# Performance work log

Hardware: AMD Instinct MI355X
Metric: run time of the kernel (lower is better)

The kernel has to match this reference:

```python
import jax, jax.numpy as jnp
import numpy as np

EPS = 1e-5

def _conv1x1(x, w, b):
    # x: [B, Cin, L], w: [Cout, Cin], b: [Cout]
    return jnp.einsum('oc,bcl->bol', w, x) + b[None, :, None]

def _bn(x, g, b):
    # BatchNorm1d in training mode: batch stats over (B, L), biased variance
    m = jnp.mean(x, axis=(0, 2), keepdims=True)
    v = jnp.var(x, axis=(0, 2), keepdims=True)
    return g[None, :, None] * (x - m) * jax.lax.rsqrt(v + EPS) + b[None, :, None]

def setup_inputs() -> dict:
    key = jax.random.key(0)
    ks = jax.random.split(key, 16)
    B, H, L, K = 32, 32, 32768, 7
    rel, im, out = H // 16, H // 8, H // 4          # 2, 4, 8
    cat = (1 + K) * rel                              # 16
    w = lambda k, shape: jax.random.normal(k, shape, jnp.float32) * 0.1
    return {
        'x': jax.random.normal(ks[0], (B, H, L), jnp.float32),
        'w_phi': w(ks[1], (rel, H)),  'b_phi': w(ks[2], (rel,)),
        'w_psi': w(ks[3], (rel, H)),  'b_psi': w(ks[4], (rel,)),
        'w_beta': w(ks[5], (out, H)), 'b_beta': w(ks[6], (out,)),
        'w_cw1': w(ks[7], (im, cat)), 'b_cw1': w(ks[8], (im,)),
        'w_cw2': w(ks[9], (out, im)), 'b_cw2': w(ks[10], (out,)),
        'w_out': w(ks[11], (H, out)), 'b_out': w(ks[12], (H,)),
        'g_cat': jnp.ones((cat,), jnp.float32),  'be_cat': jnp.zeros((cat,), jnp.float32),
        'g_im': jnp.ones((im,), jnp.float32),    'be_im': jnp.zeros((im,), jnp.float32),
        'g_aggr': jnp.ones((out,), jnp.float32), 'be_aggr': jnp.zeros((out,), jnp.float32),
        'g_hid': jnp.ones((H,), jnp.float32),    'be_hid': jnp.zeros((H,), jnp.float32),
        'kernel_size': 7,
    }

def reference(x, w_phi, b_phi, w_psi, b_psi, w_beta, b_beta,
              w_cw1, b_cw1, w_cw2, b_cw2, w_out, b_out,
              g_cat, be_cat, g_im, be_im, g_aggr, be_aggr, g_hid, be_hid,
              kernel_size):
    B, H, L = x.shape
    phi = _conv1x1(x, w_phi, b_phi)                       # [B, rel, L]
    psi = _conv1x1(x, w_psi, b_psi)                       # [B, rel, L]
    p = kernel_size // 2
    psi_pad = jnp.pad(psi, ((0, 0), (0, 0), (p, p)))
    # F.unfold with kernel (k,1): channel index = c*k + j -> stack kernel axis after channel
    psi_unf = jnp.stack([psi_pad[:, :, j:j + L] for j in range(kernel_size)], axis=2)
    psi_unf = psi_unf.reshape(B, psi.shape[1] * kernel_size, L)   # [B, rel*k, L]
    h = jnp.concatenate([phi, psi_unf], axis=1)           # [B, (1+k)*rel, L]
    h = jax.nn.relu(_bn(h, g_cat, be_cat))
    h = _conv1x1(h, w_cw1, b_cw1)
    h = jax.nn.relu(_bn(h, g_im, be_im))
    weight = _conv1x1(h, w_cw2, b_cw2)                    # [B, out, L]
    beta = _conv1x1(x, w_beta, b_beta)                    # [B, out, L]
    aggr = jax.nn.relu(_bn(weight * beta, g_aggr, be_aggr))
    y = x + _conv1x1(aggr, w_out, b_out)
    return jax.nn.relu(_bn(y, g_hid, be_hid))
```

## Files before the change

### kernel.cpp

```cpp
#include <hip/hip_runtime.h>
#include <math.h>

#define Bn 32
#define Hc 32
#define Ln 32768
#define RELC 2
#define IMC 4
#define OC 8
#define CATC 16
#define KS 7
#define NPOS (Bn*Ln)
#define TPB 256
#define VPT 4
#define PPB (TPB*VPT)
#define TILES (Ln/PPB)
#define NBLK (Bn*TILES)
#define NSLOT 8
#define SSTR 128

#define iS_PHI  0
#define iSS_PHI 2
#define iS_PSI  4
#define iSS_PSI 6
#define iS_T    8
#define iSS_T   12
#define iS_AP   16
#define iSS_AP  24
#define iS_Y    32
#define iSS_Y   64
#define bPF  0
#define bPFS 6
#define bQL  12
#define bQLS 18
#define NBST 24

#define FMA4(A,S,V) { A.x=fmaf((S),(V).x,A.x); A.y=fmaf((S),(V).y,A.y); A.z=fmaf((S),(V).z,A.z); A.w=fmaf((S),(V).w,A.w); }

__device__ inline float4 affrelu(float4 v, float a, float d){
    float4 r;
    r.x=fmaxf(fmaf(a,v.x,d),0.f); r.y=fmaxf(fmaf(a,v.y,d),0.f);
    r.z=fmaxf(fmaf(a,v.z,d),0.f); r.w=fmaxf(fmaf(a,v.w,d),0.f);
    return r;
}
__device__ inline double wredd(double v){
    #pragma unroll
    for (int o=32;o>0;o>>=1) v += __shfl_down(v,o,64);
    return v;
}
__device__ inline float wredf(float v){
    #pragma unroll
    for (int o=32;o>0;o>>=1) v += __shfl_down(v,o,64);
    return v;
}
__device__ inline void atomAddD(double* p, double v){ unsafeAtomicAdd(p, v); }

__global__ void __launch_bounds__(TPB) k1(
    const float* __restrict__ x,
    const float* __restrict__ w_phi, const float* __restrict__ b_phi,
    const float* __restrict__ w_psi, const float* __restrict__ b_psi,
    const float* __restrict__ w_beta,const float* __restrict__ b_beta,
    float* __restrict__ phi, float* __restrict__ psi, float* __restrict__ beta,
    double* __restrict__ stats, double* __restrict__ bstats)
{
    __shared__ __align__(16) float wl[Hc*12 + 12];
    __shared__ double rbuf[4][8];
    const int tid = threadIdx.x;
    for (int i = tid; i < Hc*12; i += TPB) {
        int h = i/12, j = i%12;
        float v;
        if (j < 2)      v = w_phi[j*Hc + h];
        else if (j < 4) v = w_psi[(j-2)*Hc + h];
        else            v = w_beta[(j-4)*Hc + h];
        wl[h*12 + j] = v;
    }
    if (tid < 12)
        wl[Hc*12+tid] = (tid<2) ? b_phi[tid] : (tid<4) ? b_psi[tid-2] : b_beta[tid-4];
    __syncthreads();

    const int b    = blockIdx.x / TILES;
    const int tile = blockIdx.x % TILES;
    const int l0   = tile*PPB + tid*VPT;
    double* st = stats + (size_t)(blockIdx.x & (NSLOT-1))*SSTR;

    float4 acc[12];
    #pragma unroll
    for (int j=0;j<12;++j){ float bb = wl[Hc*12+j]; acc[j]=make_float4(bb,bb,bb,bb); }

    const float* xb = x + (size_t)b*Hc*Ln + l0;
    #pragma unroll 4
    for (int h=0; h<Hc; ++h) {
        const float4 xv = *(const float4*)(xb + (size_t)h*Ln);
        const float4 w0 = *(const float4*)(&wl[h*12+0]);
        const float4 w1 = *(const float4*)(&wl[h*12+4]);
        const float4 w2 = *(const float4*)(&wl[h*12+8]);
        FMA4(acc[0],w0.x,xv); FMA4(acc[1],w0.y,xv); FMA4(acc[2],w0.z,xv); FMA4(acc[3],w0.w,xv);
        FMA4(acc[4],w1.x,xv); FMA4(acc[5],w1.y,xv); FMA4(acc[6],w1.z,xv); FMA4(acc[7],w1.w,xv);
        FMA4(acc[8],w2.x,xv); FMA4(acc[9],w2.y,xv); FMA4(acc[10],w2.z,xv); FMA4(acc[11],w2.w,xv);
    }
    #pragma unroll
    for (int c=0;c<RELC;++c) *(float4*)(phi + ((size_t)(b*RELC+c))*Ln + l0) = acc[c];
    #pragma unroll
    for (int c=0;c<RELC;++c) *(float4*)(psi + ((size_t)(b*RELC+c))*Ln + l0) = acc[2+c];
    #pragma unroll
    for (int o=0;o<OC;++o)   *(float4*)(beta + ((size_t)(b*OC+o))*Ln + l0)  = acc[4+o];

    double vals[8];
    #pragma unroll
    for (int c=0;c<2;++c){
        float4 v = acc[c];
        vals[c]   = (double)v.x+v.y+v.z+v.w;
        vals[2+c] = (double)v.x*v.x+(double)v.y*v.y+(double)v.z*v.z+(double)v.w*v.w;
        float4 u = acc[2+c];
        vals[4+c] = (double)u.x+u.y+u.z+u.w;
        vals[6+c] = (double)u.x*u.x+(double)u.y*u.y+(double)u.z*u.z+(double)u.w*u.w;
    }
    if (tile==0 || tile==TILES-1) {
        #pragma unroll
        for (int c=0;c<2;++c){
            const float pv[4] = {acc[2+c].x, acc[2+c].y, acc[2+c].z, acc[2+c].w};
            #pragma unroll
            for (int e=0;e<4;++e){
                int le = l0+e;
                if (le < 3) {
                    atomAddD(&bstats[bPF +c*3+le], (double)pv[e]);
                    atomAddD(&bstats[bPFS+c*3+le], (double)pv[e]*pv[e]);
                }
                if (le >= Ln-3) {
                    int i = le-(Ln-3);
                    atomAddD(&bstats[bQL +c*3+i], (double)pv[e]);
                    atomAddD(&bstats[bQLS+c*3+i], (double)pv[e]*pv[e]);
                }
            }
        }
    }
    const int lane=tid&63, wid=tid>>6;
    #pragma unroll
    for (int i=0;i<8;++i){ double r=wredd(vals[i]); if(lane==0) rbuf[wid][i]=r; }
    __syncthreads();
    if (tid<8) atomAddD(&st[iS_PHI+tid], rbuf[0][tid]+rbuf[1][tid]+rbuf[2][tid]+rbuf[3][tid]);
}

#define CAT_AFFINE(aCat,dCat)                                                              \
    if (tid < CATC){                                                                       \
        int ch=tid; double S=0,SS=0;                                                       \
        if (ch<2){                                                                         \
            for (int s=0;s<NSLOT;++s){ S+=stats[(size_t)s*SSTR+iS_PHI+ch]; SS+=stats[(size_t)s*SSTR+iSS_PHI+ch]; } \
        } else {                                                                           \
            int c=(ch-2)/KS, j=(ch-2)%KS, d=j-KS/2;                                        \
            for (int s=0;s<NSLOT;++s){ S+=stats[(size_t)s*SSTR+iS_PSI+c]; SS+=stats[(size_t)s*SSTR+iSS_PSI+c]; }   \
            if (d>0) for (int i=0;i<d;++i)   { S-=bstats[bPF+c*3+i];  SS-=bstats[bPFS+c*3+i]; } \
            if (d<0) for (int i=3+d;i<3;++i) { S-=bstats[bQL+c*3+i];  SS-=bstats[bQLS+c*3+i]; } \
        }                                                                                  \
        double m=S/N, v=SS/N-m*m, inv=1.0/sqrt(v+1e-5);                                    \
        aCat[ch]=(float)(g_cat[ch]*inv);                                                   \
        dCat[ch]=be_cat[ch]-(float)(m*inv*g_cat[ch]);                                      \
    }

#define STAGE_PSI(psiT)                                                                    \
    _Pragma("unroll")                                                                      \
    for (int c=0;c<2;++c)                                                                  \
        for (int idx=tid; idx<1032; idx+=TPB) {                                            \
            int l = lb - 3 + idx;                                                          \
            psiT[c][idx] = (l>=0 && l<Ln && idx<1030) ? psi[((size_t)(b*RELC+c))*Ln + l] : 0.f; \
        }

#define COMPUTE_T(tacc,aCat,dCat,w1s,b1s,psiT)                                             \
    _Pragma("unroll")                                                                      \
    for (int o=0;o<IMC;++o){ float bb=b1s[o]; tacc[o]=make_float4(bb,bb,bb,bb); }          \
    _Pragma("unroll")                                                                      \
    for (int c=0;c<RELC;++c){                                                              \
        float4 pv = *(const float4*)(phi + ((size_t)(b*RELC+c))*Ln + lb + li);             \
        float4 hv = affrelu(pv, aCat[c], dCat[c]);                                         \
        _Pragma("unroll")                                                                  \
        for (int o=0;o<IMC;++o) FMA4(tacc[o], w1s[o*CATC+c], hv);                          \
    }                                                                                      \
    _Pragma("unroll")                                                                      \
    for (int c=0;c<RELC;++c){                                                              \
        float4 A  = *(const float4*)&psiT[c][li];                                          \
        float4 Bv = *(const float4*)&psiT[c][li+4];                                        \
        float4 Cv = *(const float4*)&psiT[c][li+8];                                        \
        float pr[12] = {A.x,A.y,A.z,A.w, Bv.x,Bv.y,Bv.z,Bv.w, Cv.x,Cv.y,Cv.z,Cv.w};        \
        _Pragma("unroll")                                                                  \
        for (int j=0;j<KS;++j){                                                            \
            int ch = 2 + c*KS + j;                                                         \
            float a=aCat[ch], d=dCat[ch];                                                  \
            float4 hv;                                                                     \
            hv.x=fmaxf(fmaf(a,pr[j+0],d),0.f);                                             \
            hv.y=fmaxf(fmaf(a,pr[j+1],d),0.f);                                             \
            hv.z=fmaxf(fmaf(a,pr[j+2],d),0.f);                                             \
            hv.w=fmaxf(fmaf(a,pr[j+3],d),0.f);                                             \
            _Pragma("unroll")                                                              \
            for (int o=0;o<IMC;++o) FMA4(tacc[o], w1s[o*CATC+ch], hv);                     \
        }                                                                                  \
    }

__global__ void __launch_bounds__(TPB) k3t(
    const float* __restrict__ phi, const float* __restrict__ psi,
    const float* __restrict__ w_cw1, const float* __restrict__ b_cw1,
    const float* __restrict__ g_cat, const float* __restrict__ be_cat,
    double* __restrict__ stats, const double* __restrict__ bstats)
{
    __shared__ float aCat[CATC], dCat[CATC];
    __shared__ float w1s[IMC*CATC], b1s[IMC];
    __shared__ __align__(16) float psiT[2][1032];
    __shared__ double rbuf[4][8];
    const int tid = threadIdx.x;
    const double N = (double)NPOS;
    const int b    = blockIdx.x / TILES;
    const int tile = blockIdx.x % TILES;
    const int lb   = tile*PPB;
    const int li   = tid*VPT;
    double* st = stats + (size_t)(blockIdx.x & (NSLOT-1))*SSTR;

    CAT_AFFINE(aCat,dCat)
    if (tid < IMC*CATC) w1s[tid] = w_cw1[tid];
    if (tid < IMC)      b1s[tid] = b_cw1[tid];
    STAGE_PSI(psiT)
    __syncthreads();

    float4 tacc[IMC];
    COMPUTE_T(tacc,aCat,dCat,w1s,b1s,psiT)

    double vals[8];
    #pragma unroll
    for (int o=0;o<IMC;++o){
        float4 v = tacc[o];
        vals[o]   = (double)v.x+v.y+v.z+v.w;
        vals[4+o] = (double)v.x*v.x+(double)v.y*v.y+(double)v.z*v.z+(double)v.w*v.w;
    }
    const int lane=tid&63, wid=tid>>6;
    #pragma unroll
    for (int i=0;i<8;++i){ double r=wredd(vals[i]); if(lane==0) rbuf[wid][i]=r; }
    __syncthreads();
    if (tid<8) atomAddD(&st[iS_T+tid], rbuf[0][tid]+rbuf[1][tid]+rbuf[2][tid]+rbuf[3][tid]);
}

__global__ void __launch_bounds__(TPB) k5a(
    const float* __restrict__ phi, const float* __restrict__ psi,
    const float* __restrict__ beta,
    const float* __restrict__ w_cw1, const float* __restrict__ b_cw1,
    const float* __restrict__ w_cw2, const float* __restrict__ b_cw2,
    const float* __restrict__ g_cat, const float* __restrict__ be_cat,
    const float* __restrict__ g_im,  const float* __restrict__ be_im,
    double* __restrict__ stats, const double* __restrict__ bstats)
{
    __shared__ float aCat[CATC], dCat[CATC], aIm[IMC], dIm[IMC];
    __shared__ float w1s[IMC*CATC], b1s[IMC], w2s[OC*IMC], b2s[OC];
    __shared__ __align__(16) float psiT[2][1032];
    __shared__ double rbuf[4][16];
    const int tid = threadIdx.x;
    const double N = (double)NPOS;
    const int b    = blockIdx.x / TILES;
    const int tile = blockIdx.x % TILES;
    const int lb   = tile*PPB;
    const int li   = tid*VPT;
    double* st = stats + (size_t)(blockIdx.x & (NSLOT-1))*SSTR;

    CAT_AFFINE(aCat,dCat)
    if (tid>=32 && tid<32+IMC){
        int i=tid-32; double S=0,SS=0;
        for (int s=0;s<NSLOT;++s){ S+=stats[(size_t)s*SSTR+iS_T+i]; SS+=stats[(size_t)s*SSTR+iSS_T+i]; }
        double m=S/N, v=SS/N-m*m, inv=1.0/sqrt(v+1e-5);
        aIm[i]=(float)(g_im[i]*inv); dIm[i]=be_im[i]-(float)(m*inv*g_im[i]);
    }
    if (tid < IMC*CATC) w1s[tid] = w_cw1[tid];
    if (tid < IMC)      b1s[tid] = b_cw1[tid];
    if (tid>=64 && tid<64+OC*IMC) w2s[tid-64]=w_cw2[tid-64];
    if (tid>=96 && tid<96+OC)     b2s[tid-96]=b_cw2[tid-96];
    STAGE_PSI(psiT)
    __syncthreads();

    float4 tacc[IMC];
    COMPUTE_T(tacc,aCat,dCat,w1s,b1s,psiT)

    double vals[16];
    {
        float4 h2[IMC];
        #pragma unroll
        for (int i=0;i<IMC;++i) h2[i]=affrelu(tacc[i],aIm[i],dIm[i]);
        #pragma unroll
        for (int o=0;o<OC;++o){
            float bb=b2s[o];
            float4 w=make_float4(bb,bb,bb,bb);
            #pragma unroll
            for (int i=0;i<IMC;++i) FMA4(w,w2s[o*IMC+i],h2[i]);
            float4 bv = *(const float4*)(beta + ((size_t)(b*OC+o))*Ln + lb + li);
            float4 av; av.x=w.x*bv.x; av.y=w.y*bv.y; av.z=w.z*bv.z; av.w=w.w*bv.w;
            vals[o]   = (double)av.x+av.y+av.z+av.w;
            vals[8+o] = (double)av.x*av.x+(double)av.y*av.y+(double)av.z*av.z+(double)av.w*av.w;
        }
    }
    const int lane=tid&63, wid=tid>>6;
    #pragma unroll
    for (int i=0;i<16;++i){ double r=wredd(vals[i]); if(lane==0) rbuf[wid][i]=r; }
    __syncthreads();
    if (tid<16) atomAddD(&st[iS_AP+tid], rbuf[0][tid]+rbuf[1][tid]+rbuf[2][tid]+rbuf[3][tid]);
}

__global__ void __launch_bounds__(TPB) k7y(
    const float* __restrict__ x,
    const float* __restrict__ phi, const float* __restrict__ psi,
    const float* __restrict__ beta,
    const float* __restrict__ w_cw1, const float* __restrict__ b_cw1,
    const float* __restrict__ w_cw2, const float* __restrict__ b_cw2,
    const float* __restrict__ w_out, const float* __restrict__ b_out,
    const float* __restrict__ g_cat, const float* __restrict__ be_cat,
    const float* __restrict__ g_im,  const float* __restrict__ be_im,
    const float* __restrict__ g_ag,  const float* __restrict__ be_ag,
    double* __restrict__ stats, const double* __restrict__ bstats)
{
    __shared__ float aCat[CATC], dCat[CATC], aIm[IMC], dIm[IMC], aAg[OC], dAg[OC];
    __shared__ float w1s[IMC*CATC], b1s[IMC], w2s[OC*IMC], b2s[OC];
    __shared__ __align__(16) float wos[Hc*OC];
    __shared__ float bos[Hc];
    __shared__ __align__(16) float psiT[2][1032];
    __shared__ float fredS[Hc][4], fredQ[Hc][4];
    const int tid = threadIdx.x;
    const double N = (double)NPOS;
    const int b    = blockIdx.x / TILES;
    const int tile = blockIdx.x % TILES;
    const int lb   = tile*PPB;
    const int li   = tid*VPT;
    double* st = stats + (size_t)(blockIdx.x & (NSLOT-1))*SSTR;

    CAT_AFFINE(aCat,dCat)
    if (tid>=32 && tid<32+IMC){
        int i=tid-32; double S=0,SS=0;
        for (int s=0;s<NSLOT;++s){ S+=stats[(size_t)s*SSTR+iS_T+i]; SS+=stats[(size_t)s*SSTR+iSS_T+i]; }
        double m=S/N, v=SS/N-m*m, inv=1.0/sqrt(v+1e-5);
        aIm[i]=(float)(g_im[i]*inv); dIm[i]=be_im[i]-(float)(m*inv*g_im[i]);
    }
    if (tid>=48 && tid<48+OC){
        int o=tid-48; double S=0,SS=0;
        for (int s=0;s<NSLOT;++s){ S+=stats[(size_t)s*SSTR+iS_AP+o]; SS+=stats[(size_t)s*SSTR+iSS_AP+o]; }
        double m=S/N, v=SS/N-m*m, inv=1.0/sqrt(v+1e-5);
        aAg[o]=(float)(g_ag[o]*inv); dAg[o]=be_ag[o]-(float)(m*inv*g_ag[o]);
    }
    if (tid < IMC*CATC) w1s[tid] = w_cw1[tid];
    if (tid < IMC)      b1s[tid] = b_cw1[tid];
    if (tid>=64 && tid<64+OC*IMC) w2s[tid-64]=w_cw2[tid-64];
    if (tid>=96 && tid<96+OC)     b2s[tid-96]=b_cw2[tid-96];
    wos[tid] = w_out[tid];
    if (tid>=128 && tid<128+Hc) bos[tid-128]=b_out[tid-128];
    STAGE_PSI(psiT)
    __syncthreads();

    float4 tacc[IMC];
    COMPUTE_T(tacc,aCat,dCat,w1s,b1s,psiT)

    float4 ag[OC];
    {
        float4 h2[IMC];
        #pragma unroll
        for (int i=0;i<IMC;++i) h2[i]=affrelu(tacc[i],aIm[i],dIm[i]);
        #pragma unroll
        for (int o=0;o<OC;++o){
            float bb=b2s[o];
            float4 w=make_float4(bb,bb,bb,bb);
            #pragma unroll
            for (int i=0;i<IMC;++i) FMA4(w,w2s[o*IMC+i],h2[i]);
            float4 bv = *(const float4*)(beta + ((size_t)(b*OC+o))*Ln + lb + li);
            float4 av; av.x=w.x*bv.x; av.y=w.y*bv.y; av.z=w.z*bv.z; av.w=w.w*bv.w;
            ag[o]=affrelu(av, aAg[o], dAg[o]);
        }
    }
    const int lane=tid&63, wid=tid>>6;
    const float* xb = x + (size_t)b*Hc*Ln + lb + li;
    #pragma unroll 4
    for (int h=0;h<Hc;++h){
        float4 y = *(const float4*)(xb + (size_t)h*Ln);
        float bb=bos[h]; y.x+=bb; y.y+=bb; y.z+=bb; y.w+=bb;
        #pragma unroll
        for (int o=0;o<OC;++o) FMA4(y, wos[h*OC+o], ag[o]);
        float fs=y.x+y.y+y.z+y.w;
        float fq=y.x*y.x+y.y*y.y+y.z*y.z+y.w*y.w;
        fs=wredf(fs); fq=wredf(fq);
        if (lane==0){ fredS[h][wid]=fs; fredQ[h][wid]=fq; }
    }
    __syncthreads();
    if (tid<Hc){
        double s=(double)fredS[tid][0]+fredS[tid][1]+fredS[tid][2]+fredS[tid][3];
        double q=(double)fredQ[tid][0]+fredQ[tid][1]+fredQ[tid][2]+fredQ[tid][3];
        atomAddD(&st[iS_Y +tid], s);
        atomAddD(&st[iSS_Y+tid], q);
    }
}

__global__ void __launch_bounds__(TPB) k9o(
    const float* __restrict__ x,
    const float* __restrict__ phi, const float* __restrict__ psi,
    const float* __restrict__ beta,
    const float* __restrict__ w_cw1, const float* __restrict__ b_cw1,
    const float* __restrict__ w_cw2, const float* __restrict__ b_cw2,
    const float* __restrict__ w_out, const float* __restrict__ b_out,
    const float* __restrict__ g_cat, const float* __restrict__ be_cat,
    const float* __restrict__ g_im,  const float* __restrict__ be_im,
    const float* __restrict__ g_ag,  const float* __restrict__ be_ag,
    const float* __restrict__ g_hid, const float* __restrict__ be_hid,
    float* __restrict__ out,
    const double* __restrict__ stats, const double* __restrict__ bstats)
{
    __shared__ float aCat[CATC], dCat[CATC], aIm[IMC], dIm[IMC], aAg[OC], dAg[OC];
    __shared__ float aHid[Hc], dHid[Hc];
    __shared__ float w1s[IMC*CATC], b1s[IMC], w2s[OC*IMC], b2s[OC];
    __shared__ __align__(16) float wos[Hc*OC];
    __shared__ float bos[Hc];
    __shared__ __align__(16) float psiT[2][1032];
    const int tid = threadIdx.x;
    const double N = (double)NPOS;
    const int b    = blockIdx.x / TILES;
    const int tile = blockIdx.x % TILES;
    const int lb   = tile*PPB;
    const int li   = tid*VPT;

    CAT_AFFINE(aCat,dCat)
    if (tid>=32 && tid<32+IMC){
        int i=tid-32; double S=0,SS=0;
        for (int s=0;s<NSLOT;++s){ S+=stats[(size_t)s*SSTR+iS_T+i]; SS+=stats[(size_t)s*SSTR+iSS_T+i]; }
        double m=S/N, v=SS/N-m*m, inv=1.0/sqrt(v+1e-5);
        aIm[i]=(float)(g_im[i]*inv); dIm[i]=be_im[i]-(float)(m*inv*g_im[i]);
    }
    if (tid>=48 && tid<48+OC){
        int o=tid-48; double S=0,SS=0;
        for (int s=0;s<NSLOT;++s){ S+=stats[(size_t)s*SSTR+iS_AP+o]; SS+=stats[(size_t)s*SSTR+iSS_AP+o]; }
        double m=S/N, v=SS/N-m*m, inv=1.0/sqrt(v+1e-5);
        aAg[o]=(float)(g_ag[o]*inv); dAg[o]=be_ag[o]-(float)(m*inv*g_ag[o]);
    }
    if (tid>=160 && tid<160+Hc){
        int h=tid-160; double S=0,SS=0;
        for (int s=0;s<NSLOT;++s){ S+=stats[(size_t)s*SSTR+iS_Y+h]; SS+=stats[(size_t)s*SSTR+iSS_Y+h]; }
        double m=S/N, v=SS/N-m*m, inv=1.0/sqrt(v+1e-5);
        aHid[h]=(float)(g_hid[h]*inv); dHid[h]=be_hid[h]-(float)(m*inv*g_hid[h]);
    }
    if (tid < IMC*CATC) w1s[tid] = w_cw1[tid];
    if (tid < IMC)      b1s[tid] = b_cw1[tid];
    if (tid>=64 && tid<64+OC*IMC) w2s[tid-64]=w_cw2[tid-64];
    if (tid>=96 && tid<96+OC)     b2s[tid-96]=b_cw2[tid-96];
    wos[tid] = w_out[tid];
    if (tid>=128 && tid<128+Hc) bos[tid-128]=b_out[tid-128];
    STAGE_PSI(psiT)
    __syncthreads();

    float4 tacc[IMC];
    COMPUTE_T(tacc,aCat,dCat,w1s,b1s,psiT)

    float4 ag[OC];
    {
        float4 h2[IMC];
        #pragma unroll
        for (int i=0;i<IMC;++i) h2[i]=affrelu(tacc[i],aIm[i],dIm[i]);
        #pragma unroll
        for (int o=0;o<OC;++o){
            float bb=b2s[o];
            float4 w=make_float4(bb,bb,bb,bb);
            #pragma unroll
            for (int i=0;i<IMC;++i) FMA4(w,w2s[o*IMC+i],h2[i]);
            float4 bv = *(const float4*)(beta + ((size_t)(b*OC+o))*Ln + lb + li);
            float4 av; av.x=w.x*bv.x; av.y=w.y*bv.y; av.z=w.z*bv.z; av.w=w.w*bv.w;
            ag[o]=affrelu(av, aAg[o], dAg[o]);
        }
    }
    const float* xb = x + (size_t)b*Hc*Ln + lb + li;
    float* ob = out + (size_t)b*Hc*Ln + lb + li;
    #pragma unroll 4
    for (int h=0;h<Hc;++h){
        float4 y = *(const float4*)(xb + (size_t)h*Ln);
        float bb=bos[h]; y.x+=bb; y.y+=bb; y.z+=bb; y.w+=bb;
        #pragma unroll
        for (int o=0;o<OC;++o) FMA4(y, wos[h*OC+o], ag[o]);
        *(float4*)(ob + (size_t)h*Ln) = affrelu(y, aHid[h], dHid[h]);
    }
}

extern "C" void kernel_launch(void* const* d_in, const int* in_sizes, int n_in,
                              void* d_out, int out_size, void* d_ws, size_t ws_size,
                              hipStream_t stream)
{
    const float* x     =(const float*)d_in[0];
    const float* w_phi =(const float*)d_in[1];  const float* b_phi =(const float*)d_in[2];
    const float* w_psi =(const float*)d_in[3];  const float* b_psi =(const float*)d_in[4];
    const float* w_beta=(const float*)d_in[5];  const float* b_beta=(const float*)d_in[6];
    const float* w_cw1 =(const float*)d_in[7];  const float* b_cw1 =(const float*)d_in[8];
    const float* w_cw2 =(const float*)d_in[9];  const float* b_cw2 =(const float*)d_in[10];
    const float* w_out =(const float*)d_in[11]; const float* b_out =(const float*)d_in[12];
    const float* g_cat =(const float*)d_in[13]; const float* be_cat=(const float*)d_in[14];
    const float* g_im  =(const float*)d_in[15]; const float* be_im =(const float*)d_in[16];
    const float* g_ag  =(const float*)d_in[17]; const float* be_ag =(const float*)d_in[18];
    const float* g_hid =(const float*)d_in[19]; const float* be_hid=(const float*)d_in[20];

    double* stats  = (double*)d_ws;
    double* bstats = stats + (size_t)NSLOT*SSTR;
    float*  fbase  = (float*)((char*)d_ws + 16384);
    float* phi  = fbase;
    float* psi  = phi + (size_t)Bn*RELC*Ln;
    float* beta = psi + (size_t)Bn*RELC*Ln;

    hipMemsetAsync(d_ws, 0, ((size_t)NSLOT*SSTR + NBST)*sizeof(double), stream);
    k1 <<<NBLK, TPB, 0, stream>>>(x, w_phi,b_phi, w_psi,b_psi, w_beta,b_beta,
                                  phi,psi,beta, stats,bstats);
    k3t<<<NBLK, TPB, 0, stream>>>(phi,psi, w_cw1,b_cw1, g_cat,be_cat, stats,bstats);
    k5a<<<NBLK, TPB, 0, stream>>>(phi,psi,beta, w_cw1,b_cw1, w_cw2,b_cw2,
                                  g_cat,be_cat, g_im,be_im, stats,bstats);
    k7y<<<NBLK, TPB, 0, stream>>>(x, phi,psi,beta, w_cw1,b_cw1, w_cw2,b_cw2, w_out,b_out,
                                  g_cat,be_cat, g_im,be_im, g_ag,be_ag, stats,bstats);
    k9o<<<NBLK, TPB, 0, stream>>>(x, phi,psi,beta, w_cw1,b_cw1, w_cw2,b_cw2, w_out,b_out,
                                  g_cat,be_cat, g_im,be_im, g_ag,be_ag, g_hid,be_hid,
                                  (float*)d_out, stats,bstats);
}
```

Measured before the change: 195.7 us.

## Split k7y/k9o across two hidden-channel halves, add nontemporal output stores

k7y and k9o now launch twice as many blocks, and each block handles 16 of the 32 hidden channels for its tile. Each half recomputes the shared cat/im/aggr chain (psi staging, conv1, conv2 times beta) redundantly. Stat slots grow from 8 to 16 to spread the atomics, the workspace offset grows to match, and both kernels get launch_bounds with 8 blocks per SM. Output stores use nontemporal hints. The aim is more parallelism and occupancy in the x-streaming kernels, paid for by duplicated phi/psi/beta reads and duplicated compute.

```diff
diff --git a/kernel.cpp b/kernel.cpp
--- a/kernel.cpp
+++ b/kernel.cpp
@@ -15,7 +15,9 @@
 #define PPB (TPB*VPT)
 #define TILES (Ln/PPB)
 #define NBLK (Bn*TILES)
-#define NSLOT 8
+#define NBLKH (NBLK*2)
+#define HHALF 16
+#define NSLOT 16
 #define SSTR 128
 
 #define iS_PHI  0
@@ -53,6 +55,11 @@
     return v;
 }
 __device__ inline void atomAddD(double* p, double v){ unsafeAtomicAdd(p, v); }
+typedef float f4nt __attribute__((ext_vector_type(4)));
+__device__ inline void ntstore4(float* p, float4 v){
+    union { float4 a; f4nt b; } u; u.a = v;
+    __builtin_nontemporal_store(u.b, (f4nt*)p);
+}
 
 __global__ void __launch_bounds__(TPB) k1(
     const float* __restrict__ x,
@@ -194,6 +201,37 @@
         }                                                                                  \
     }
 
+#define IM_AG_AFFINE(aIm,dIm,aAg,dAg)                                                      \
+    if (tid>=32 && tid<32+IMC){                                                            \
+        int i=tid-32; double S=0,SS=0;                                                     \
+        for (int s=0;s<NSLOT;++s){ S+=stats[(size_t)s*SSTR+iS_T+i]; SS+=stats[(size_t)s*SSTR+iSS_T+i]; } \
+        double m=S/N, v=SS/N-m*m, inv=1.0/sqrt(v+1e-5);                                    \
+        aIm[i]=(float)(g_im[i]*inv); dIm[i]=be_im[i]-(float)(m*inv*g_im[i]);               \
+    }                                                                                      \
+    if (tid>=48 && tid<48+OC){                                                             \
+        int o=tid-48; double S=0,SS=0;                                                     \
+        for (int s=0;s<NSLOT;++s){ S+=stats[(size_t)s*SSTR+iS_AP+o]; SS+=stats[(size_t)s*SSTR+iSS_AP+o]; } \
+        double m=S/N, v=SS/N-m*m, inv=1.0/sqrt(v+1e-5);                                    \
+        aAg[o]=(float)(g_ag[o]*inv); dAg[o]=be_ag[o]-(float)(m*inv*g_ag[o]);               \
+    }
+
+#define COMPUTE_AG(ag,tacc,aIm,dIm,aAg,dAg,w2s,b2s)                                        \
+    {                                                                                      \
+        float4 h2[IMC];                                                                    \
+        _Pragma("unroll")                                                                  \
+        for (int i=0;i<IMC;++i) h2[i]=affrelu(tacc[i],aIm[i],dIm[i]);                      \
+        _Pragma("unroll")                                                                  \
+        for (int o=0;o<OC;++o){                                                            \
+            float bb=b2s[o];                                                               \
+            float4 w=make_float4(bb,bb,bb,bb);                                             \
+            _Pragma("unroll")                                                              \
+            for (int i=0;i<IMC;++i) FMA4(w,w2s[o*IMC+i],h2[i]);                            \
+            float4 bv = *(const float4*)(beta + ((size_t)(b*OC+o))*Ln + lb + li);          \
+            float4 av; av.x=w.x*bv.x; av.y=w.y*bv.y; av.z=w.z*bv.z; av.w=w.w*bv.w;         \
+            ag[o]=affrelu(av, aAg[o], dAg[o]);                                             \
+        }                                                                                  \
+    }
+
 __global__ void __launch_bounds__(TPB) k3t(
     const float* __restrict__ phi, const float* __restrict__ psi,
     const float* __restrict__ w_cw1, const float* __restrict__ b_cw1,
@@ -297,7 +335,7 @@
     if (tid<16) atomAddD(&st[iS_AP+tid], rbuf[0][tid]+rbuf[1][tid]+rbuf[2][tid]+rbuf[3][tid]);
 }
 
-__global__ void __launch_bounds__(TPB) k7y(
+__global__ void __launch_bounds__(TPB, 8) k7y(
     const float* __restrict__ x,
     const float* __restrict__ phi, const float* __restrict__ psi,
     const float* __restrict__ beta,
@@ -311,82 +349,60 @@
 {
     __shared__ float aCat[CATC], dCat[CATC], aIm[IMC], dIm[IMC], aAg[OC], dAg[OC];
     __shared__ float w1s[IMC*CATC], b1s[IMC], w2s[OC*IMC], b2s[OC];
-    __shared__ __align__(16) float wos[Hc*OC];
-    __shared__ float bos[Hc];
+    __shared__ __align__(16) float wos[HHALF*OC];
+    __shared__ float bos[HHALF];
     __shared__ __align__(16) float psiT[2][1032];
-    __shared__ float fredS[Hc][4], fredQ[Hc][4];
+    __shared__ float fredS[HHALF][4], fredQ[HHALF][4];
     const int tid = threadIdx.x;
     const double N = (double)NPOS;
-    const int b    = blockIdx.x / TILES;
-    const int tile = blockIdx.x % TILES;
+    const int hs   = blockIdx.x & 1;
+    const int bidx = blockIdx.x >> 1;
+    const int h0   = hs*HHALF;
+    const int b    = bidx / TILES;
+    const int tile = bidx % TILES;
     const int lb   = tile*PPB;
     const int li   = tid*VPT;
     double* st = stats + (size_t)(blockIdx.x & (NSLOT-1))*SSTR;
 
     CAT_AFFINE(aCat,dCat)
-    if (tid>=32 && tid<32+IMC){
-        int i=tid-32; double S=0,SS=0;
-        for (int s=0;s<NSLOT;++s){ S+=stats[(size_t)s*SSTR+iS_T+i]; SS+=stats[(size_t)s*SSTR+iSS_T+i]; }
-        double m=S/N, v=SS/N-m*m, inv=1.0/sqrt(v+1e-5);
-        aIm[i]=(float)(g_im[i]*inv); dIm[i]=be_im[i]-(float)(m*inv*g_im[i]);
-    }
-    if (tid>=48 && tid<48+OC){
-        int o=tid-48; double S=0,SS=0;
-        for (int s=0;s<NSLOT;++s){ S+=stats[(size_t)s*SSTR+iS_AP+o]; SS+=stats[(size_t)s*SSTR+iSS_AP+o]; }
-        double m=S/N, v=SS/N-m*m, inv=1.0/sqrt(v+1e-5);
-        aAg[o]=(float)(g_ag[o]*inv); dAg[o]=be_ag[o]-(float)(m*inv*g_ag[o]);
-    }
+    IM_AG_AFFINE(aIm,dIm,aAg,dAg)
     if (tid < IMC*CATC) w1s[tid] = w_cw1[tid];
     if (tid < IMC)      b1s[tid] = b_cw1[tid];
     if (tid>=64 && tid<64+OC*IMC) w2s[tid-64]=w_cw2[tid-64];
     if (tid>=96 && tid<96+OC)     b2s[tid-96]=b_cw2[tid-96];
-    wos[tid] = w_out[tid];
-    if (tid>=128 && tid<128+Hc) bos[tid-128]=b_out[tid-128];
+    if (tid < HHALF*OC) wos[tid] = w_out[(size_t)(h0 + tid/OC)*OC + (tid%OC)];
+    if (tid>=128 && tid<128+HHALF) bos[tid-128]=b_out[h0 + tid-128];
     STAGE_PSI(psiT)
     __syncthreads();
 
     float4 tacc[IMC];
     COMPUTE_T(tacc,aCat,dCat,w1s,b1s,psiT)
-
     float4 ag[OC];
-    {
-        float4 h2[IMC];
-        #pragma unroll
-        for (int i=0;i<IMC;++i) h2[i]=affrelu(tacc[i],aIm[i],dIm[i]);
-        #pragma unroll
-        for (int o=0;o<OC;++o){
-            float bb=b2s[o];
-            float4 w=make_float4(bb,bb,bb,bb);
-            #pragma unroll
-            for (int i=0;i<IMC;++i) FMA4(w,w2s[o*IMC+i],h2[i]);
-            float4 bv = *(const float4*)(beta + ((size_t)(b*OC+o))*Ln + lb + li);
-            float4 av; av.x=w.x*bv.x; av.y=w.y*bv.y; av.z=w.z*bv.z; av.w=w.w*bv.w;
-            ag[o]=affrelu(av, aAg[o], dAg[o]);
-        }
-    }
+    COMPUTE_AG(ag,tacc,aIm,dIm,aAg,dAg,w2s,b2s)
+
     const int lane=tid&63, wid=tid>>6;
     const float* xb = x + (size_t)b*Hc*Ln + lb + li;
     #pragma unroll 4
-    for (int h=0;h<Hc;++h){
-        float4 y = *(const float4*)(xb + (size_t)h*Ln);
-        float bb=bos[h]; y.x+=bb; y.y+=bb; y.z+=bb; y.w+=bb;
+    for (int hh=0;hh<HHALF;++hh){
+        float4 y = *(const float4*)(xb + (size_t)(h0+hh)*Ln);
+        float bb=bos[hh]; y.x+=bb; y.y+=bb; y.z+=bb; y.w+=bb;
         #pragma unroll
-        for (int o=0;o<OC;++o) FMA4(y, wos[h*OC+o], ag[o]);
+        for (int o=0;o<OC;++o) FMA4(y, wos[hh*OC+o], ag[o]);
         float fs=y.x+y.y+y.z+y.w;
         float fq=y.x*y.x+y.y*y.y+y.z*y.z+y.w*y.w;
         fs=wredf(fs); fq=wredf(fq);
-        if (lane==0){ fredS[h][wid]=fs; fredQ[h][wid]=fq; }
-    }
-    __syncthreads();
-    if (tid<Hc){
+        if (lane==0){ fredS[hh][wid]=fs; fredQ[hh][wid]=fq; }
+    }
+    __syncthreads();
+    if (tid<HHALF){
         double s=(double)fredS[tid][0]+fredS[tid][1]+fredS[tid][2]+fredS[tid][3];
         double q=(double)fredQ[tid][0]+fredQ[tid][1]+fredQ[tid][2]+fredQ[tid][3];
-        atomAddD(&st[iS_Y +tid], s);
-        atomAddD(&st[iSS_Y+tid], q);
-    }
-}
-
-__global__ void __launch_bounds__(TPB) k9o(
+        atomAddD(&st[iS_Y +h0+tid], s);
+        atomAddD(&st[iSS_Y+h0+tid], q);
+    }
+}
+
+__global__ void __launch_bounds__(TPB, 8) k9o(
     const float* __restrict__ x,
     const float* __restrict__ phi, const float* __restrict__ psi,
     const float* __restrict__ beta,
@@ -401,74 +417,52 @@
     const double* __restrict__ stats, const double* __restrict__ bstats)
 {
     __shared__ float aCat[CATC], dCat[CATC], aIm[IMC], dIm[IMC], aAg[OC], dAg[OC];
-    __shared__ float aHid[Hc], dHid[Hc];
+    __shared__ float aHid[HHALF], dHid[HHALF];
     __shared__ float w1s[IMC*CATC], b1s[IMC], w2s[OC*IMC], b2s[OC];
-    __shared__ __align__(16) float wos[Hc*OC];
-    __shared__ float bos[Hc];
+    __shared__ __align__(16) float wos[HHALF*OC];
+    __shared__ float bos[HHALF];
     __shared__ __align__(16) float psiT[2][1032];
     const int tid = threadIdx.x;
     const double N = (double)NPOS;
-    const int b    = blockIdx.x / TILES;
-    const int tile = blockIdx.x % TILES;
+    const int hs   = blockIdx.x & 1;
+    const int bidx = blockIdx.x >> 1;
+    const int h0   = hs*HHALF;
+    const int b    = bidx / TILES;
+    const int tile = bidx % TILES;
     const int lb   = tile*PPB;
     const int li   = tid*VPT;
 
     CAT_AFFINE(aCat,dCat)
-    if (tid>=32 && tid<32+IMC){
-        int i=tid-32; double S=0,SS=0;
-        for (int s=0;s<NSLOT;++s){ S+=stats[(size_t)s*SSTR+iS_T+i]; SS+=stats[(size_t)s*SSTR+iSS_T+i]; }
-        double m=S/N, v=SS/N-m*m, inv=1.0/sqrt(v+1e-5);
-        aIm[i]=(float)(g_im[i]*inv); dIm[i]=be_im[i]-(float)(m*inv*g_im[i]);
-    }
-    if (tid>=48 && tid<48+OC){
-        int o=tid-48; double S=0,SS=0;
-        for (int s=0;s<NSLOT;++s){ S+=stats[(size_t)s*SSTR+iS_AP+o]; SS+=stats[(size_t)s*SSTR+iSS_AP+o]; }
-        double m=S/N, v=SS/N-m*m, inv=1.0/sqrt(v+1e-5);
-        aAg[o]=(float)(g_ag[o]*inv); dAg[o]=be_ag[o]-(float)(m*inv*g_ag[o]);
-    }
-    if (tid>=160 && tid<160+Hc){
-        int h=tid-160; double S=0,SS=0;
+    IM_AG_AFFINE(aIm,dIm,aAg,dAg)
+    if (tid>=160 && tid<160+HHALF){
+        int hh=tid-160, h=h0+hh; double S=0,SS=0;
         for (int s=0;s<NSLOT;++s){ S+=stats[(size_t)s*SSTR+iS_Y+h]; SS+=stats[(size_t)s*SSTR+iSS_Y+h]; }
         double m=S/N, v=SS/N-m*m, inv=1.0/sqrt(v+1e-5);
-        aHid[h]=(float)(g_hid[h]*inv); dHid[h]=be_hid[h]-(float)(m*inv*g_hid[h]);
+        aHid[hh]=(float)(g_hid[h]*inv); dHid[hh]=be_hid[h]-(float)(m*inv*g_hid[h]);
     }
     if (tid < IMC*CATC) w1s[tid] = w_cw1[tid];
     if (tid < IMC)      b1s[tid] = b_cw1[tid];
     if (tid>=64 && tid<64+OC*IMC) w2s[tid-64]=w_cw2[tid-64];
     if (tid>=96 && tid<96+OC)     b2s[tid-96]=b_cw2[tid-96];
-    wos[tid] = w_out[tid];
-    if (tid>=128 && tid<128+Hc) bos[tid-128]=b_out[tid-128];
+    if (tid < HHALF*OC) wos[tid] = w_out[(size_t)(h0 + tid/OC)*OC + (tid%OC)];
+    if (tid>=128 && tid<128+HHALF) bos[tid-128]=b_out[h0 + tid-128];
     STAGE_PSI(psiT)
     __syncthreads();
 
     float4 tacc[IMC];
     COMPUTE_T(tacc,aCat,dCat,w1s,b1s,psiT)
-
     float4 ag[OC];
-    {
-        float4 h2[IMC];
-        #pragma unroll
-        for (int i=0;i<IMC;++i) h2[i]=affrelu(tacc[i],aIm[i],dIm[i]);
-        #pragma unroll
-        for (int o=0;o<OC;++o){
-            float bb=b2s[o];
-            float4 w=make_float4(bb,bb,bb,bb);
-            #pragma unroll
-            for (int i=0;i<IMC;++i) FMA4(w,w2s[o*IMC+i],h2[i]);
-            float4 bv = *(const float4*)(beta + ((size_t)(b*OC+o))*Ln + lb + li);
-            float4 av; av.x=w.x*bv.x; av.y=w.y*bv.y; av.z=w.z*bv.z; av.w=w.w*bv.w;
-            ag[o]=affrelu(av, aAg[o], dAg[o]);
-        }
-    }
+    COMPUTE_AG(ag,tacc,aIm,dIm,aAg,dAg,w2s,b2s)
+
     const float* xb = x + (size_t)b*Hc*Ln + lb + li;
     float* ob = out + (size_t)b*Hc*Ln + lb + li;
     #pragma unroll 4
-    for (int h=0;h<Hc;++h){
-        float4 y = *(const float4*)(xb + (size_t)h*Ln);
-        float bb=bos[h]; y.x+=bb; y.y+=bb; y.z+=bb; y.w+=bb;
+    for (int hh=0;hh<HHALF;++hh){
+        float4 y = *(const float4*)(xb + (size_t)(h0+hh)*Ln);
+        float bb=bos[hh]; y.x+=bb; y.y+=bb; y.z+=bb; y.w+=bb;
         #pragma unroll
-        for (int o=0;o<OC;++o) FMA4(y, wos[h*OC+o], ag[o]);
-        *(float4*)(ob + (size_t)h*Ln) = affrelu(y, aHid[h], dHid[h]);
+        for (int o=0;o<OC;++o) FMA4(y, wos[hh*OC+o], ag[o]);
+        ntstore4(ob + (size_t)(h0+hh)*Ln, affrelu(y, aHid[hh], dHid[hh]));
     }
 }
 
@@ -490,20 +484,20 @@
 
     double* stats  = (double*)d_ws;
     double* bstats = stats + (size_t)NSLOT*SSTR;
-    float*  fbase  = (float*)((char*)d_ws + 16384);
+    float*  fbase  = (float*)((char*)d_ws + 32768);
     float* phi  = fbase;
     float* psi  = phi + (size_t)Bn*RELC*Ln;
     float* beta = psi + (size_t)Bn*RELC*Ln;
 
     hipMemsetAsync(d_ws, 0, ((size_t)NSLOT*SSTR + NBST)*sizeof(double), stream);
-    k1 <<<NBLK, TPB, 0, stream>>>(x, w_phi,b_phi, w_psi,b_psi, w_beta,b_beta,
-                                  phi,psi,beta, stats,bstats);
-    k3t<<<NBLK, TPB, 0, stream>>>(phi,psi, w_cw1,b_cw1, g_cat,be_cat, stats,bstats);
-    k5a<<<NBLK, TPB, 0, stream>>>(phi,psi,beta, w_cw1,b_cw1, w_cw2,b_cw2,
-                                  g_cat,be_cat, g_im,be_im, stats,bstats);
-    k7y<<<NBLK, TPB, 0, stream>>>(x, phi,psi,beta, w_cw1,b_cw1, w_cw2,b_cw2, w_out,b_out,
-                                  g_cat,be_cat, g_im,be_im, g_ag,be_ag, stats,bstats);
-    k9o<<<NBLK, TPB, 0, stream>>>(x, phi,psi,beta, w_cw1,b_cw1, w_cw2,b_cw2, w_out,b_out,
-                                  g_cat,be_cat, g_im,be_im, g_ag,be_ag, g_hid,be_hid,
-                                  (float*)d_out, stats,bstats);
-}
+    k1 <<<NBLK,  TPB, 0, stream>>>(x, w_phi,b_phi, w_psi,b_psi, w_beta,b_beta,
+                                   phi,psi,beta, stats,bstats);
+    k3t<<<NBLK,  TPB, 0, stream>>>(phi,psi, w_cw1,b_cw1, g_cat,be_cat, stats,bstats);
+    k5a<<<NBLK,  TPB, 0, stream>>>(phi,psi,beta, w_cw1,b_cw1, w_cw2,b_cw2,
+                                   g_cat,be_cat, g_im,be_im, stats,bstats);
+    k7y<<<NBLKH, TPB, 0, stream>>>(x, phi,psi,beta, w_cw1,b_cw1, w_cw2,b_cw2, w_out,b_out,
+                                   g_cat,be_cat, g_im,be_im, g_ag,be_ag, stats,bstats);
+    k9o<<<NBLKH, TPB, 0, stream>>>(x, phi,psi,beta, w_cw1,b_cw1, w_cw2,b_cw2, w_out,b_out,
+                                   g_cat,be_cat, g_im,be_im, g_ag,be_ag, g_hid,be_hid,
+                                   (float*)d_out, stats,bstats);
+}
```

Result: slower. 201.8 us (+3.1%).
